# Optimization experiments

Measured on AMD Instinct MI355X. Metric: run time of the kernel, lower is better.

## Reference

```python
import jax, jax.numpy as jnp
import numpy as np

B, HT, WT = 4, 256, 256        # batch, token grid h, w
WS, NH, VD = 8, 8, 128         # window_size, num_heads, values_dim==inner_dim
HD = VD // NH                  # head_dim = 16
WH, WW = HT // WS, WT // WS    # windows per axis (no padding needed)

_idx = np.array([[x, y] for x in range(WS) for y in range(WS)])
_REL = jnp.asarray(_idx[None, :, :] - _idx[:, None, :] + WS - 1)  # [64,64,2]

def _shift_masks():
    m = np.zeros((WS * WS, WS * WS), np.float32)
    s = WS * (WS // 2)
    m[-s:, :-s] = -np.inf
    m[:-s, -s:] = -np.inf
    # '(r w1) (c w2) -> (w1 r) (w2 c)'
    cm = m.reshape(WS, WS, WS, WS).transpose(1, 0, 3, 2).reshape(WS * WS, WS * WS)
    return jnp.asarray(m), jnp.asarray(cm)

_ROW_MASK, _COL_MASK = _shift_masks()

def setup_inputs() -> dict:
    key = jax.random.key(0)
    ks = jax.random.split(key, 9)
    N = HT * WT
    return {
        'embedded_values': jax.random.normal(ks[0], (B, N, VD), jnp.float32),
        'embedded_coords': jax.random.normal(ks[1], (B, N, VD), jnp.float32),
        'Wv': jax.random.normal(ks[2], (VD, 3 * VD), jnp.float32) * 0.05,
        'bv': jax.random.normal(ks[3], (3 * VD,), jnp.float32) * 0.05,
        'Wc': jax.random.normal(ks[4], (VD, 2 * VD), jnp.float32) * 0.05,
        'bc': jax.random.normal(ks[5], (2 * VD,), jnp.float32) * 0.05,
        'pos_emb': jax.random.normal(ks[6], (2 * WS - 1, 2 * WS - 1), jnp.float32),
        'Wo': jax.random.normal(ks[7], (VD, VD), jnp.float32) * 0.05,
        'bo': jax.random.normal(ks[8], (VD,), jnp.float32) * 0.05,
    }

def _to_windows(t, k):
    # b (Wh w1) (Ww w2) (e H) k -> b H Wh Ww (w1 w2) e k  (head index innermost in channel)
    t = t.reshape(B, WH, WS, WW, WS, HD, NH, k)
    t = t.transpose(0, 6, 1, 3, 2, 4, 5, 7)
    return t.reshape(B, NH, WH, WW, WS * WS, HD, k)

def reference(embedded_values, embedded_coords, Wv, bv, Wc, bc, pos_emb, Wo, bo):
    v = embedded_values @ Wv + bv              # [B, N, 3*VD]
    c = embedded_coords @ Wc + bc              # [B, N, 2*VD]
    # '(d k)' split: k innermost
    v = v.reshape(B, HT, WT, VD, 3)
    c = c.reshape(B, HT, WT, VD, 2)
    # shifted windows: roll by -window_size//2 (source never rolls back)
    v = jnp.roll(v, (-(WS // 2), -(WS // 2)), axis=(1, 2))
    c = jnp.roll(c, (-(WS // 2), -(WS // 2)), axis=(1, 2))
    v = _to_windows(v, 3)
    c = _to_windows(c, 2)
    qv, kv, vv = v[..., 0], v[..., 1], v[..., 2]
    qc, kc = c[..., 0], c[..., 1]
    dots = (jnp.einsum('bhxyie,bhxyje->bhxyij', qv, kv)
            + jnp.einsum('bhxyie,bhxyje->bhxyij', qc, kc)) / jnp.float32(HD) ** 0.5
    dots = dots + pos_emb[_REL[..., 0], _REL[..., 1]]  # relative position bias
    dots = dots.at[:, :, -1, :].add(_ROW_MASK)
    dots = dots.at[:, :, :, -1].add(_COL_MASK)
    y = jax.nn.softmax(dots, axis=-1) @ vv     # [B,NH,WH,WW,64,HD]
    # b H Wh Ww (w1 w2) e -> b (Wh w1) (Ww w2) (H e)
    y = y.reshape(B, NH, WH, WW, WS, WS, HD).transpose(0, 2, 4, 3, 5, 1, 6)
    y = y.reshape(B, HT * WT, VD)
    return y @ Wo + bo
```

## Files before the change

### kernel.cpp

```cpp
#include <hip/hip_runtime.h>


typedef __bf16 bf16_t;
typedef __bf16 bf16x4 __attribute__((ext_vector_type(4)));
typedef __bf16 bf16x8 __attribute__((ext_vector_type(8)));
typedef float f32x4 __attribute__((ext_vector_type(4)));

#define SMEM_BYTES 53248

__global__ __launch_bounds__(512) void prep_weights_k(
    const float* __restrict__ Wv, const float* __restrict__ Wc,
    const float* __restrict__ Wo, bf16_t* __restrict__ wsW) {
  int g = blockIdx.x * 512 + threadIdx.x;
  int frag = g >> 9, within = g & 511;
  int l = within >> 3, j = within & 7;
  int cc = l & 15;
  int kin_off = ((l >> 4) << 3) + j;
  float val;
  if (frag < 160) {
    int h = frag / 20, fi = frag % 20;
    int type = fi >> 2, ks = fi & 3;
    int kin = ks * 32 + kin_off;
    if (type == 0)      val = Wv[kin * 384 + (cc * 8 + h) * 3];
    else if (type == 1) val = Wv[kin * 384 + (cc * 8 + h) * 3 + 1];
    else if (type == 2) val = Wc[kin * 256 + (cc * 8 + h) * 2];
    else if (type == 3) val = Wc[kin * 256 + (cc * 8 + h) * 2 + 1];
    else                val = Wv[kin * 384 + (cc * 8 + h) * 3 + 2];
    wsW[g] = (bf16_t)val;
  } else {
    int f = frag - 160, nt = f >> 2, ks = f & 3;
    int kin = ks * 32 + kin_off;
    wsW[g] = (bf16_t)Wo[kin * 128 + nt * 16 + cc];
  }
}

__global__ __launch_bounds__(512) void swin_fused_k(
    const float* __restrict__ gxv, const float* __restrict__ gxc,
    const float* __restrict__ bv, const float* __restrict__ bc,
    const float* __restrict__ pos_g, const float* __restrict__ bo,
    const bf16_t* __restrict__ wsW, float* __restrict__ out) {
  extern __shared__ char smem[];
  bf16_t* XV = (bf16_t*)(smem);
  bf16_t* XC = (bf16_t*)(smem + 17408);
  bf16_t* Y  = (bf16_t*)(smem + 34816);
  float*  POS = (float*)(smem + 52224);

  const int tid = threadIdx.x;
  const int l = tid & 63;
  const int w = tid >> 6;
  const int col16 = l & 15;
  const int q = l >> 4;

  const int bid = blockIdx.x;
  const int b = bid >> 10;
  const int rem = bid & 1023;
  const int wy = rem >> 5, wx = rem & 31;
  const bool lastRow = (wy == 31), lastCol = (wx == 31);

  if (tid < 225) POS[tid] = pos_g[tid];

  const int h = w;
  float bqv_[4], bkv_[4], bqc_[4], bkc_[4];
#pragma unroll
  for (int r = 0; r < 4; ++r) {
    const int ev = q * 4 + r;
    bqv_[r] = bv[(ev * 8 + h) * 3 + 0];
    bkv_[r] = bv[(ev * 8 + h) * 3 + 1];
    bqc_[r] = bc[(ev * 8 + h) * 2 + 0];
    bkc_[r] = bc[(ev * 8 + h) * 2 + 1];
  }
  const float bvv = bv[(col16 * 8 + h) * 3 + 2];

  {
    const int t = tid >> 3, qq = tid & 7;
    const int rs = ((wy << 3) + (t >> 3) + 4) & 255;
    const int cs = ((wx << 3) + (t & 7) + 4) & 255;
    const size_t base = ((size_t)b * 65536 + (size_t)rs * 256 + (size_t)cs) * 128;
    const float4* pv = (const float4*)(gxv + base);
    const float4* pc = (const float4*)(gxc + base);
#pragma unroll
    for (int i = 0; i < 4; ++i) {
      float4 a = pv[i * 8 + qq];
      bf16x4 pk; pk[0]=(bf16_t)a.x; pk[1]=(bf16_t)a.y; pk[2]=(bf16_t)a.z; pk[3]=(bf16_t)a.w;
      *(bf16x4*)(XV + t * 136 + (i * 8 + qq) * 4) = pk;
      float4 c = pc[i * 8 + qq];
      bf16x4 qk; qk[0]=(bf16_t)c.x; qk[1]=(bf16_t)c.y; qk[2]=(bf16_t)c.z; qk[3]=(bf16_t)c.w;
      *(bf16x4*)(XC + t * 136 + (i * 8 + qq) * 4) = qk;
    }
  }
  __syncthreads();

  const bf16_t* wsH = wsW + h * 10240;

  bf16x8 xf[4][4];
#pragma unroll
  for (int ni = 0; ni < 4; ++ni)
#pragma unroll
    for (int ks = 0; ks < 4; ++ks)
      xf[ni][ks] = *(const bf16x8*)(XV + (ni * 16 + col16) * 136 + ks * 32 + q * 8);
  f32x4 qa[4] = {}, ka[4] = {}, va[4] = {};
#pragma unroll
  for (int ks = 0; ks < 4; ++ks) {
    bf16x8 wq = *(const bf16x8*)(wsH + (0  + ks) * 512 + l * 8);
    bf16x8 wk = *(const bf16x8*)(wsH + (4  + ks) * 512 + l * 8);
    bf16x8 wv = *(const bf16x8*)(wsH + (16 + ks) * 512 + l * 8);
#pragma unroll
    for (int t4 = 0; t4 < 4; ++t4) {
      qa[t4] = __builtin_amdgcn_mfma_f32_16x16x32_bf16(wq, xf[t4][ks], qa[t4], 0, 0, 0);
      ka[t4] = __builtin_amdgcn_mfma_f32_16x16x32_bf16(wk, xf[t4][ks], ka[t4], 0, 0, 0);
      va[t4] = __builtin_amdgcn_mfma_f32_16x16x32_bf16(xf[t4][ks], wv, va[t4], 0, 0, 0);
    }
  }
  bf16x8 aV[2];
#pragma unroll
  for (int ks2 = 0; ks2 < 2; ++ks2)
#pragma unroll
    for (int jj = 0; jj < 8; ++jj)
      aV[ks2][jj] = (bf16_t)(va[2 * ks2 + (jj >> 2)][jj & 3] + bvv);

#pragma unroll
  for (int ni = 0; ni < 4; ++ni)
#pragma unroll
    for (int ks = 0; ks < 4; ++ks)
      xf[ni][ks] = *(const bf16x8*)(XC + (ni * 16 + col16) * 136 + ks * 32 + q * 8);
  f32x4 qc[4] = {}, kc[4] = {};
#pragma unroll
  for (int ks = 0; ks < 4; ++ks) {
    bf16x8 wq = *(const bf16x8*)(wsH + (8  + ks) * 512 + l * 8);
    bf16x8 wk = *(const bf16x8*)(wsH + (12 + ks) * 512 + l * 8);
#pragma unroll
    for (int t4 = 0; t4 < 4; ++t4) {
      qc[t4] = __builtin_amdgcn_mfma_f32_16x16x32_bf16(wq, xf[t4][ks], qc[t4], 0, 0, 0);
      kc[t4] = __builtin_amdgcn_mfma_f32_16x16x32_bf16(wk, xf[t4][ks], kc[t4], 0, 0, 0);
    }
  }
  bf16x8 aK[4], bQ[4];
#pragma unroll
  for (int m = 0; m < 4; ++m) {
#pragma unroll
    for (int r = 0; r < 4; ++r) {
      aK[m][r]     = (bf16_t)(ka[m][r] + bkv_[r]);
      aK[m][4 + r] = (bf16_t)(kc[m][r] + bkc_[r]);
      bQ[m][r]     = (bf16_t)(qa[m][r] + bqv_[r]);
      bQ[m][4 + r] = (bf16_t)(qc[m][r] + bqc_[r]);
    }
  }

  f32x4 s[4][4];
  const f32x4 zz = {0.f, 0.f, 0.f, 0.f};
#pragma unroll
  for (int mj = 0; mj < 4; ++mj)
#pragma unroll
    for (int ni = 0; ni < 4; ++ni)
      s[mj][ni] = __builtin_amdgcn_mfma_f32_16x16x32_bf16(aK[mj], bQ[ni], zz, 0, 0, 0);

  float inv[4];
#pragma unroll
  for (int ni = 0; ni < 4; ++ni) {
    const int i = ni * 16 + col16;
    const int ix = i >> 3, iy = i & 7;
    float m = -3.4e38f;
#pragma unroll
    for (int mj = 0; mj < 4; ++mj)
#pragma unroll
      for (int r = 0; r < 4; ++r) {
        const int j = mj * 16 + q * 4 + r;
        float v = s[mj][ni][r] * 0.25f +
                  POS[((j >> 3) - ix + 7) * 15 + ((j & 7) - iy + 7)];
        if (lastRow && ((i ^ j) & 32)) v = -1e30f;
        if (lastCol && ((i ^ j) & 4))  v = -1e30f;
        s[mj][ni][r] = v;
        m = fmaxf(m, v);
      }
    m = fmaxf(m, __shfl_xor(m, 16, 64));
    m = fmaxf(m, __shfl_xor(m, 32, 64));
    float sum = 0.f;
#pragma unroll
    for (int mj = 0; mj < 4; ++mj)
#pragma unroll
      for (int r = 0; r < 4; ++r) {
        float e = __expf(s[mj][ni][r] - m);
        s[mj][ni][r] = e;
        sum += e;
      }
    sum += __shfl_xor(sum, 16, 64);
    sum += __shfl_xor(sum, 32, 64);
    inv[ni] = __builtin_amdgcn_rcpf(sum);
  }

  f32x4 oacc[4] = {};
#pragma unroll
  for (int ks2 = 0; ks2 < 2; ++ks2) {
#pragma unroll
    for (int ni = 0; ni < 4; ++ni) {
      bf16x8 bP;
#pragma unroll
      for (int jj = 0; jj < 8; ++jj)
        bP[jj] = (bf16_t)(s[2 * ks2 + (jj >> 2)][ni][jj & 3] * inv[ni]);
      oacc[ni] = __builtin_amdgcn_mfma_f32_16x16x32_bf16(aV[ks2], bP, oacc[ni], 0, 0, 0);
    }
  }
#pragma unroll
  for (int ni = 0; ni < 4; ++ni) {
    bf16x4 pk;
#pragma unroll
    for (int r = 0; r < 4; ++r) pk[r] = (bf16_t)(oacc[ni][r]);
    *(bf16x4*)(Y + (ni * 16 + col16) * 136 + h * 16 + q * 4) = pk;
  }
  __syncthreads();

#pragma unroll
  for (int mi = 0; mi < 4; ++mi)
#pragma unroll
    for (int ks = 0; ks < 4; ++ks)
      xf[mi][ks] = *(const bf16x8*)(Y + (mi * 16 + col16) * 136 + ks * 32 + q * 8);
  f32x4 acc[4] = {};
#pragma unroll
  for (int ks = 0; ks < 4; ++ks) {
    bf16x8 bWo = *(const bf16x8*)(wsW + 81920 + (w * 4 + ks) * 512 + l * 8);
#pragma unroll
    for (int mi = 0; mi < 4; ++mi)
      acc[mi] = __builtin_amdgcn_mfma_f32_16x16x32_bf16(xf[mi][ks], bWo, acc[mi], 0, 0, 0);
  }
  const int o = w * 16 + col16;
  const float bias = bo[o];
  const int rg0 = wy << 3, cg0 = wx << 3;
#pragma unroll
  for (int mi = 0; mi < 4; ++mi)
#pragma unroll
    for (int r = 0; r < 4; ++r) {
      const int t = mi * 16 + q * 4 + r;
      const int rg = rg0 + (t >> 3), cg = cg0 + (t & 7);
      out[(((size_t)b * 65536 + (size_t)rg * 256 + (size_t)cg) << 7) + o] =
          acc[mi][r] + bias;
    }
}

extern "C" void kernel_launch(void* const* d_in, const int* in_sizes, int n_in,
                              void* d_out, int out_size, void* d_ws, size_t ws_size,
                              hipStream_t stream) {
  const float* gxv = (const float*)d_in[0];
  const float* gxc = (const float*)d_in[1];
  const float* Wv  = (const float*)d_in[2];
  const float* bv  = (const float*)d_in[3];
  const float* Wc  = (const float*)d_in[4];
  const float* bc  = (const float*)d_in[5];
  const float* pe  = (const float*)d_in[6];
  const float* Wo  = (const float*)d_in[7];
  const float* bo  = (const float*)d_in[8];
  float* out = (float*)d_out;
  bf16_t* wsW = (bf16_t*)d_ws;

  hipFuncSetAttribute((const void*)swin_fused_k,
                      hipFuncAttributeMaxDynamicSharedMemorySize, SMEM_BYTES);
  prep_weights_k<<<192, 512, 0, stream>>>(Wv, Wc, Wo, wsW);
  swin_fused_k<<<4096, 512, SMEM_BYTES, stream>>>(gxv, gxc, bv, bc, pe, bo, wsW, out);
}
```

Before: 398.6 us.

## Alias LDS buffers, fold scale and biases, drop softmax max, vectorize output stores

Reuses the XV shared buffer for the attention output to shrink LDS and requests 6 blocks per CU via launch bounds. The 1/sqrt(d) scale is folded into the Q weights and biases, and the biases and positional terms are preloaded into MFMA accumulators. The softmax max-subtraction is removed, and normalization is applied after the PV matmul. Output is computed transposed so each lane writes float4, giving coalesced stores. Dropping the max risks overflow for large scores, and the register and occupancy trade-off may vary.

Result: slower. 471.9 us (+18.4%).

```diff
diff --git a/kernel.cpp b/kernel.cpp
--- a/kernel.cpp
+++ b/kernel.cpp
@@ -6,7 +6,7 @@
 typedef __bf16 bf16x8 __attribute__((ext_vector_type(8)));
 typedef float f32x4 __attribute__((ext_vector_type(4)));
 
-#define SMEM_BYTES 53248
+#define SMEM_BYTES 35840
 
 __global__ __launch_bounds__(512) void prep_weights_k(
     const float* __restrict__ Wv, const float* __restrict__ Wc,
@@ -21,9 +21,9 @@
     int h = frag / 20, fi = frag % 20;
     int type = fi >> 2, ks = fi & 3;
     int kin = ks * 32 + kin_off;
-    if (type == 0)      val = Wv[kin * 384 + (cc * 8 + h) * 3];
+    if (type == 0)      val = 0.25f * Wv[kin * 384 + (cc * 8 + h) * 3];
     else if (type == 1) val = Wv[kin * 384 + (cc * 8 + h) * 3 + 1];
-    else if (type == 2) val = Wc[kin * 256 + (cc * 8 + h) * 2];
+    else if (type == 2) val = 0.25f * Wc[kin * 256 + (cc * 8 + h) * 2];
     else if (type == 3) val = Wc[kin * 256 + (cc * 8 + h) * 2 + 1];
     else                val = Wv[kin * 384 + (cc * 8 + h) * 3 + 2];
     wsW[g] = (bf16_t)val;
@@ -34,7 +34,7 @@
   }
 }
 
-__global__ __launch_bounds__(512) void swin_fused_k(
+__global__ __launch_bounds__(512, 6) void swin_fused_k(
     const float* __restrict__ gxv, const float* __restrict__ gxc,
     const float* __restrict__ bv, const float* __restrict__ bc,
     const float* __restrict__ pos_g, const float* __restrict__ bo,
@@ -42,8 +42,8 @@
   extern __shared__ char smem[];
   bf16_t* XV = (bf16_t*)(smem);
   bf16_t* XC = (bf16_t*)(smem + 17408);
-  bf16_t* Y  = (bf16_t*)(smem + 34816);
-  float*  POS = (float*)(smem + 52224);
+  bf16_t* Y  = (bf16_t*)(smem);
+  float*  POS = (float*)(smem + 34816);
 
   const int tid = threadIdx.x;
   const int l = tid & 63;
@@ -60,16 +60,6 @@
   if (tid < 225) POS[tid] = pos_g[tid];
 
   const int h = w;
-  float bqv_[4], bkv_[4], bqc_[4], bkc_[4];
-#pragma unroll
-  for (int r = 0; r < 4; ++r) {
-    const int ev = q * 4 + r;
-    bqv_[r] = bv[(ev * 8 + h) * 3 + 0];
-    bkv_[r] = bv[(ev * 8 + h) * 3 + 1];
-    bqc_[r] = bc[(ev * 8 + h) * 2 + 0];
-    bkc_[r] = bc[(ev * 8 + h) * 2 + 1];
-  }
-  const float bvv = bv[(col16 * 8 + h) * 3 + 2];
 
   {
     const int t = tid >> 3, qq = tid & 7;
@@ -92,148 +82,184 @@
 
   const bf16_t* wsH = wsW + h * 10240;
 
-  bf16x8 xf[4][4];
-#pragma unroll
-  for (int ni = 0; ni < 4; ++ni)
-#pragma unroll
-    for (int ks = 0; ks < 4; ++ks)
-      xf[ni][ks] = *(const bf16x8*)(XV + (ni * 16 + col16) * 136 + ks * 32 + q * 8);
-  f32x4 qa[4] = {}, ka[4] = {}, va[4] = {};
-#pragma unroll
-  for (int ks = 0; ks < 4; ++ks) {
-    bf16x8 wq = *(const bf16x8*)(wsH + (0  + ks) * 512 + l * 8);
-    bf16x8 wk = *(const bf16x8*)(wsH + (4  + ks) * 512 + l * 8);
-    bf16x8 wv = *(const bf16x8*)(wsH + (16 + ks) * 512 + l * 8);
-#pragma unroll
-    for (int t4 = 0; t4 < 4; ++t4) {
-      qa[t4] = __builtin_amdgcn_mfma_f32_16x16x32_bf16(wq, xf[t4][ks], qa[t4], 0, 0, 0);
-      ka[t4] = __builtin_amdgcn_mfma_f32_16x16x32_bf16(wk, xf[t4][ks], ka[t4], 0, 0, 0);
-      va[t4] = __builtin_amdgcn_mfma_f32_16x16x32_bf16(xf[t4][ks], wv, va[t4], 0, 0, 0);
-    }
-  }
-  bf16x8 aV[2];
-#pragma unroll
-  for (int ks2 = 0; ks2 < 2; ++ks2)
-#pragma unroll
-    for (int jj = 0; jj < 8; ++jj)
-      aV[ks2][jj] = (bf16_t)(va[2 * ks2 + (jj >> 2)][jj & 3] + bvv);
-
-#pragma unroll
-  for (int ni = 0; ni < 4; ++ni)
-#pragma unroll
-    for (int ks = 0; ks < 4; ++ks)
-      xf[ni][ks] = *(const bf16x8*)(XC + (ni * 16 + col16) * 136 + ks * 32 + q * 8);
-  f32x4 qc[4] = {}, kc[4] = {};
-#pragma unroll
-  for (int ks = 0; ks < 4; ++ks) {
-    bf16x8 wq = *(const bf16x8*)(wsH + (8  + ks) * 512 + l * 8);
-    bf16x8 wk = *(const bf16x8*)(wsH + (12 + ks) * 512 + l * 8);
-#pragma unroll
-    for (int t4 = 0; t4 < 4; ++t4) {
-      qc[t4] = __builtin_amdgcn_mfma_f32_16x16x32_bf16(wq, xf[t4][ks], qc[t4], 0, 0, 0);
-      kc[t4] = __builtin_amdgcn_mfma_f32_16x16x32_bf16(wk, xf[t4][ks], kc[t4], 0, 0, 0);
-    }
-  }
-  bf16x8 aK[4], bQ[4];
-#pragma unroll
-  for (int m = 0; m < 4; ++m) {
-#pragma unroll
-    for (int r = 0; r < 4; ++r) {
-      aK[m][r]     = (bf16_t)(ka[m][r] + bkv_[r]);
-      aK[m][4 + r] = (bf16_t)(kc[m][r] + bkc_[r]);
-      bQ[m][r]     = (bf16_t)(qa[m][r] + bqv_[r]);
-      bQ[m][4 + r] = (bf16_t)(qc[m][r] + bqc_[r]);
-    }
-  }
-
-  f32x4 s[4][4];
-  const f32x4 zz = {0.f, 0.f, 0.f, 0.f};
-#pragma unroll
-  for (int mj = 0; mj < 4; ++mj)
-#pragma unroll
-    for (int ni = 0; ni < 4; ++ni)
-      s[mj][ni] = __builtin_amdgcn_mfma_f32_16x16x32_bf16(aK[mj], bQ[ni], zz, 0, 0, 0);
-
-  float inv[4];
+  bf16x8 aK[4], bQ[4], aV[2];
+  {
+    f32x4 qa[4], ka[4], va[4];
+    {
+      f32x4 initQ, initK, initV;
+#pragma unroll
+      for (int r = 0; r < 4; ++r) {
+        const int ev = q * 4 + r;
+        initQ[r] = 0.25f * bv[(ev * 8 + h) * 3 + 0];
+        initK[r] = bv[(ev * 8 + h) * 3 + 1];
+      }
+      const float bvv = bv[(col16 * 8 + h) * 3 + 2];
+      initV[0] = bvv; initV[1] = bvv; initV[2] = bvv; initV[3] = bvv;
+#pragma unroll
+      for (int t4 = 0; t4 < 4; ++t4) { qa[t4] = initQ; ka[t4] = initK; va[t4] = initV; }
+    }
+#pragma unroll
+    for (int ks = 0; ks < 4; ++ks) {
+      bf16x8 xk[4];
+#pragma unroll
+      for (int t4 = 0; t4 < 4; ++t4)
+        xk[t4] = *(const bf16x8*)(XV + (t4 * 16 + col16) * 136 + ks * 32 + q * 8);
+      bf16x8 wq = *(const bf16x8*)(wsH + (0  + ks) * 512 + l * 8);
+      bf16x8 wk = *(const bf16x8*)(wsH + (4  + ks) * 512 + l * 8);
+      bf16x8 wv = *(const bf16x8*)(wsH + (16 + ks) * 512 + l * 8);
+#pragma unroll
+      for (int t4 = 0; t4 < 4; ++t4) {
+        qa[t4] = __builtin_amdgcn_mfma_f32_16x16x32_bf16(wq, xk[t4], qa[t4], 0, 0, 0);
+        ka[t4] = __builtin_amdgcn_mfma_f32_16x16x32_bf16(wk, xk[t4], ka[t4], 0, 0, 0);
+        va[t4] = __builtin_amdgcn_mfma_f32_16x16x32_bf16(xk[t4], wv, va[t4], 0, 0, 0);
+      }
+    }
+#pragma unroll
+    for (int ks2 = 0; ks2 < 2; ++ks2)
+#pragma unroll
+      for (int jj = 0; jj < 8; ++jj)
+        aV[ks2][jj] = (bf16_t)(va[2 * ks2 + (jj >> 2)][jj & 3]);
+#pragma unroll
+    for (int m = 0; m < 4; ++m)
+#pragma unroll
+      for (int r = 0; r < 4; ++r) {
+        aK[m][r] = (bf16_t)ka[m][r];
+        bQ[m][r] = (bf16_t)qa[m][r];
+      }
+  }
+  {
+    f32x4 cacc[4];
+    {
+      f32x4 initQC;
+#pragma unroll
+      for (int r = 0; r < 4; ++r) initQC[r] = 0.25f * bc[((q * 4 + r) * 8 + h) * 2 + 0];
+#pragma unroll
+      for (int t4 = 0; t4 < 4; ++t4) cacc[t4] = initQC;
+    }
+#pragma unroll
+    for (int ks = 0; ks < 4; ++ks) {
+      bf16x8 xk[4];
+#pragma unroll
+      for (int t4 = 0; t4 < 4; ++t4)
+        xk[t4] = *(const bf16x8*)(XC + (t4 * 16 + col16) * 136 + ks * 32 + q * 8);
+      bf16x8 wq = *(const bf16x8*)(wsH + (8 + ks) * 512 + l * 8);
+#pragma unroll
+      for (int t4 = 0; t4 < 4; ++t4)
+        cacc[t4] = __builtin_amdgcn_mfma_f32_16x16x32_bf16(wq, xk[t4], cacc[t4], 0, 0, 0);
+    }
+#pragma unroll
+    for (int m = 0; m < 4; ++m)
+#pragma unroll
+      for (int r = 0; r < 4; ++r) bQ[m][4 + r] = (bf16_t)cacc[m][r];
+  }
+  {
+    f32x4 cacc[4];
+    {
+      f32x4 initKC;
+#pragma unroll
+      for (int r = 0; r < 4; ++r) initKC[r] = bc[((q * 4 + r) * 8 + h) * 2 + 1];
+#pragma unroll
+      for (int t4 = 0; t4 < 4; ++t4) cacc[t4] = initKC;
+    }
+#pragma unroll
+    for (int ks = 0; ks < 4; ++ks) {
+      bf16x8 xk[4];
+#pragma unroll
+      for (int t4 = 0; t4 < 4; ++t4)
+        xk[t4] = *(const bf16x8*)(XC + (t4 * 16 + col16) * 136 + ks * 32 + q * 8);
+      bf16x8 wk = *(const bf16x8*)(wsH + (12 + ks) * 512 + l * 8);
+#pragma unroll
+      for (int t4 = 0; t4 < 4; ++t4)
+        cacc[t4] = __builtin_amdgcn_mfma_f32_16x16x32_bf16(wk, xk[t4], cacc[t4], 0, 0, 0);
+    }
+#pragma unroll
+    for (int m = 0; m < 4; ++m)
+#pragma unroll
+      for (int r = 0; r < 4; ++r) aK[m][4 + r] = (bf16_t)cacc[m][r];
+  }
+  __syncthreads();
+
 #pragma unroll
   for (int ni = 0; ni < 4; ++ni) {
     const int i = ni * 16 + col16;
-    const int ix = i >> 3, iy = i & 7;
-    float m = -3.4e38f;
+    const int pb = ((q >> 1) - (i >> 3) + 7) * 15 + ((q & 1) << 2) - (i & 7) + 7;
+    f32x4 sv[4];
 #pragma unroll
     for (int mj = 0; mj < 4; ++mj)
 #pragma unroll
+      for (int r = 0; r < 4; ++r)
+        sv[mj][r] = POS[pb + mj * 30 + r];
+#pragma unroll
+    for (int mj = 0; mj < 4; ++mj)
+      sv[mj] = __builtin_amdgcn_mfma_f32_16x16x32_bf16(aK[mj], bQ[ni], sv[mj], 0, 0, 0);
+    if (lastRow) {
+#pragma unroll
+      for (int mj = 0; mj < 4; ++mj)
+#pragma unroll
+        for (int r = 0; r < 4; ++r)
+          if ((i ^ (mj * 16 + q * 4 + r)) & 32) sv[mj][r] = -1e30f;
+    }
+    if (lastCol) {
+#pragma unroll
+      for (int mj = 0; mj < 4; ++mj)
+#pragma unroll
+        for (int r = 0; r < 4; ++r)
+          if ((i ^ (mj * 16 + q * 4 + r)) & 4) sv[mj][r] = -1e30f;
+    }
+    float sum = 0.f;
+#pragma unroll
+    for (int mj = 0; mj < 4; ++mj)
+#pragma unroll
       for (int r = 0; r < 4; ++r) {
-        const int j = mj * 16 + q * 4 + r;
-        float v = s[mj][ni][r] * 0.25f +
-                  POS[((j >> 3) - ix + 7) * 15 + ((j & 7) - iy + 7)];
-        if (lastRow && ((i ^ j) & 32)) v = -1e30f;
-        if (lastCol && ((i ^ j) & 4))  v = -1e30f;
-        s[mj][ni][r] = v;
-        m = fmaxf(m, v);
-      }
-    m = fmaxf(m, __shfl_xor(m, 16, 64));
-    m = fmaxf(m, __shfl_xor(m, 32, 64));
-    float sum = 0.f;
-#pragma unroll
-    for (int mj = 0; mj < 4; ++mj)
-#pragma unroll
-      for (int r = 0; r < 4; ++r) {
-        float e = __expf(s[mj][ni][r] - m);
-        s[mj][ni][r] = e;
+        float e = __expf(sv[mj][r]);
+        sv[mj][r] = e;
         sum += e;
       }
     sum += __shfl_xor(sum, 16, 64);
     sum += __shfl_xor(sum, 32, 64);
-    inv[ni] = __builtin_amdgcn_rcpf(sum);
-  }
-
-  f32x4 oacc[4] = {};
-#pragma unroll
-  for (int ks2 = 0; ks2 < 2; ++ks2) {
+    const float inv = __builtin_amdgcn_rcpf(sum);
+    bf16x8 bP0, bP1;
+#pragma unroll
+    for (int jj = 0; jj < 8; ++jj) {
+      bP0[jj] = (bf16_t)sv[(jj >> 2)][jj & 3];
+      bP1[jj] = (bf16_t)sv[2 + (jj >> 2)][jj & 3];
+    }
+    const f32x4 zz = {0.f, 0.f, 0.f, 0.f};
+    f32x4 o = __builtin_amdgcn_mfma_f32_16x16x32_bf16(aV[0], bP0, zz, 0, 0, 0);
+    o = __builtin_amdgcn_mfma_f32_16x16x32_bf16(aV[1], bP1, o, 0, 0, 0);
+    bf16x4 pk;
+#pragma unroll
+    for (int r = 0; r < 4; ++r) pk[r] = (bf16_t)(o[r] * inv);
+    *(bf16x4*)(Y + i * 136 + h * 16 + q * 4) = pk;
+  }
+  __syncthreads();
+
+  {
+    f32x4 acc[4] = {};
+#pragma unroll
+    for (int ks = 0; ks < 4; ++ks) {
+      bf16x8 woA = *(const bf16x8*)(wsW + 81920 + (w * 4 + ks) * 512 + l * 8);
+#pragma unroll
+      for (int ni = 0; ni < 4; ++ni) {
+        bf16x8 yf = *(const bf16x8*)(Y + (ni * 16 + col16) * 136 + ks * 32 + q * 8);
+        acc[ni] = __builtin_amdgcn_mfma_f32_16x16x32_bf16(woA, yf, acc[ni], 0, 0, 0);
+      }
+    }
+    const float4 bo4 = *(const float4*)(bo + w * 16 + q * 4);
+    const int rg0 = wy << 3, cg0 = wx << 3;
 #pragma unroll
     for (int ni = 0; ni < 4; ++ni) {
-      bf16x8 bP;
-#pragma unroll
-      for (int jj = 0; jj < 8; ++jj)
-        bP[jj] = (bf16_t)(s[2 * ks2 + (jj >> 2)][ni][jj & 3] * inv[ni]);
-      oacc[ni] = __builtin_amdgcn_mfma_f32_16x16x32_bf16(aV[ks2], bP, oacc[ni], 0, 0, 0);
-    }
-  }
-#pragma unroll
-  for (int ni = 0; ni < 4; ++ni) {
-    bf16x4 pk;
-#pragma unroll
-    for (int r = 0; r < 4; ++r) pk[r] = (bf16_t)(oacc[ni][r]);
-    *(bf16x4*)(Y + (ni * 16 + col16) * 136 + h * 16 + q * 4) = pk;
-  }
-  __syncthreads();
-
-#pragma unroll
-  for (int mi = 0; mi < 4; ++mi)
-#pragma unroll
-    for (int ks = 0; ks < 4; ++ks)
-      xf[mi][ks] = *(const bf16x8*)(Y + (mi * 16 + col16) * 136 + ks * 32 + q * 8);
-  f32x4 acc[4] = {};
-#pragma unroll
-  for (int ks = 0; ks < 4; ++ks) {
-    bf16x8 bWo = *(const bf16x8*)(wsW + 81920 + (w * 4 + ks) * 512 + l * 8);
-#pragma unroll
-    for (int mi = 0; mi < 4; ++mi)
-      acc[mi] = __builtin_amdgcn_mfma_f32_16x16x32_bf16(xf[mi][ks], bWo, acc[mi], 0, 0, 0);
-  }
-  const int o = w * 16 + col16;
-  const float bias = bo[o];
-  const int rg0 = wy << 3, cg0 = wx << 3;
-#pragma unroll
-  for (int mi = 0; mi < 4; ++mi)
-#pragma unroll
-    for (int r = 0; r < 4; ++r) {
-      const int t = mi * 16 + q * 4 + r;
+      const int t = ni * 16 + col16;
       const int rg = rg0 + (t >> 3), cg = cg0 + (t & 7);
-      out[(((size_t)b * 65536 + (size_t)rg * 256 + (size_t)cg) << 7) + o] =
-          acc[mi][r] + bias;
-    }
+      float4 st;
+      st.x = acc[ni][0] + bo4.x;
+      st.y = acc[ni][1] + bo4.y;
+      st.z = acc[ni][2] + bo4.z;
+      st.w = acc[ni][3] + bo4.w;
+      *(float4*)(out + ((size_t)b * 65536 + (size_t)rg * 256 + (size_t)cg) * 128 +
+                 w * 16 + q * 4) = st;
+    }
+  }
 }
 
 extern "C" void kernel_launch(void* const* d_in, const int* in_sizes, int n_in,
```
